# Performance work log

Hardware: AMD Instinct MI355X
Metric: run time of the kernel (lower is better)

## Reference

```python
import jax, jax.numpy as jnp
import numpy as np

N_PTS = 100000
C_IN, C_OUT, K = 16, 32, 3
B, D, H, W = 2, 32, 128, 128


def setup_inputs() -> dict:
    key = jax.random.key(0)
    kf, kw, kb, kz, ky, kx = jax.random.split(key, 6)
    features = jax.random.normal(kf, (N_PTS, C_IN), dtype=jnp.float32)
    coords = jnp.stack([
        jax.random.randint(kb, (N_PTS,), 0, B),
        jax.random.randint(kz, (N_PTS,), 0, D),
        jax.random.randint(ky, (N_PTS,), 0, H),
        jax.random.randint(kx, (N_PTS,), 0, W),
    ], axis=1).astype(jnp.int32)
    weight = jax.random.normal(kw, (K ** 3, C_IN, C_OUT), dtype=jnp.float32) * 0.01
    bias = jnp.zeros((C_OUT,), dtype=jnp.float32)
    return {"features": features, "coords": coords, "weight": weight, "bias": bias,
            "batch_size": B, "d_sp": D, "h_sp": H, "w_sp": W}


def reference(features, coords, weight, bias, batch_size, d_sp, h_sp, w_sp):
    # Scatter sparse voxel features into dense grid (B, C_in, D, H, W).
    n, c_in = features.shape
    c_out = weight.shape[2]
    k = K
    b, z, y, x = coords[:, 0], coords[:, 1], coords[:, 2], coords[:, 3]
    dense = jnp.zeros((batch_size, c_in, d_sp, h_sp, w_sp), dtype=features.dtype)
    dense = dense.at[b, :, z, y, x].set(features)  # (N,) advanced idx -> rows of (N, C_in)
    # Conv3d: torch copies weight.view(C_out, C_in, k, k, k) -> OIDHW kernel.
    kernel = weight.reshape(c_out, c_in, k, k, k)
    out = jax.lax.conv_general_dilated(
        dense, kernel,
        window_strides=(1, 1, 1),
        padding=[(1, 1), (1, 1), (1, 1)],
        dimension_numbers=("NCDHW", "OIDHW", "NCDHW"))
    out = jax.nn.relu(out + bias[None, :, None, None, None])
    # Dense equivalent of the torch nonzero-gather (which has data-dependent
    # shape): return the full dense activated grid (B, C_out, D, H, W).
    return out
```

## Files before the change

### kernel.cpp

```cpp
#include <hip/hip_runtime.h>

#define CIN   16
#define COUT  32
#define BATCH 2
#define DSP   32
#define HSP   128
#define WSP   128

#define TZ 4
#define TY 8
#define TX 16
#define NTZ 8
#define NTY 16
#define NTX 8
#define NTILES (BATCH*NTZ*NTY*NTX)
#define PZ 6
#define PY 10
#define PX 18
#define PVOX (PZ*PY*PX)
#define HALFU (PVOX*8)
#define BIN_CAP 128
#define NPAIR 14

typedef __bf16 bf16x8 __attribute__((ext_vector_type(8)));
typedef float  f32x4  __attribute__((ext_vector_type(4)));

__global__ void k_prep(const int4* __restrict__ coords, int n, int nbDedup,
                       int* __restrict__ map,
                       const float* __restrict__ w, __bf16* __restrict__ wpack) {
    if ((int)blockIdx.x < nbDedup) {
        int p = blockIdx.x * 256 + threadIdx.x;
        if (p >= n) return;
        int4 c = coords[p];
        int vox = ((c.x*DSP + c.y)*HSP + c.z)*WSP + c.w;
        atomicMax(&map[vox], p);
    } else {
        int i = (blockIdx.x - nbDedup) * 256 + threadIdx.x;
        if (i >= NPAIR*2*64*8) return;
        int j = i & 7, l = (i>>3) & 63, h = (i>>9) & 1, p = i >> 10;
        int tap = 2*p + ((l>>4)>>1);
        int co  = h*16 + (l & 15);
        int ci  = ((l>>4)&1)*8 + j;
        float v = (tap < 27) ? w[(co*CIN + ci)*27 + tap] : 0.0f;
        wpack[i] = (__bf16)v;
    }
}

__global__ void k_bin(const int4* __restrict__ coords, const int* __restrict__ map,
                      int* __restrict__ binCnt, int* __restrict__ bins, int n) {
    int p = blockIdx.x * 256 + threadIdx.x;
    if (p >= n) return;
    int4 c = coords[p];
    int vox = ((c.x*DSP + c.y)*HSP + c.z)*WSP + c.w;
    if (map[vox] != p) return;
    int tile = ((c.x*NTZ + (c.y>>2))*NTY + (c.z>>3))*NTX + (c.w>>4);
    int slot = atomicAdd(&binCnt[tile], 1);
    if (slot < BIN_CAP) bins[tile*BIN_CAP + slot] = p;
}

__global__ __launch_bounds__(256, 3) void k_conv(
    const float* __restrict__ feat, const int4* __restrict__ coords,
    const __bf16* __restrict__ wpack, const float* __restrict__ bias,
    const int* __restrict__ binCnt, const int* __restrict__ bins,
    float* __restrict__ out)
{
    __shared__ __align__(16) ushort patch[2*HALFU];
    __shared__ int ldsNt[27], ldsCnt[27], ldsPre[27];

    int tile = blockIdx.x;
    int txi = tile & 7;
    int tyi = (tile >> 3) & 15;
    int tzi = (tile >> 7) & 7;
    int b   = tile >> 10;
    int z0 = tzi*TZ, y0 = tyi*TY, x0 = txi*TX;

    int tid  = threadIdx.x;
    int lane = tid & 63, wave = tid >> 6;

    if (tid < 27) {
        int dz = tid/9 - 1, dy = (tid/3)%3 - 1, dx = tid%3 - 1;
        int nz = tzi+dz, ny = tyi+dy, nx = txi+dx;
        bool ok = (unsigned)nz < NTZ && (unsigned)ny < NTY && (unsigned)nx < NTX;
        int nt = ((b*NTZ + nz)*NTY + ny)*NTX + nx;
        ldsNt[tid]  = ok ? nt : 0;
        int c = ok ? binCnt[nt] : 0;
        ldsCnt[tid] = c > BIN_CAP ? BIN_CAP : c;
    }

    uint4* p4 = (uint4*)patch;
    for (int i = tid; i < 2*HALFU/8; i += 256) p4[i] = make_uint4(0,0,0,0);

    bf16x8 wf[NPAIR][2];
    #pragma unroll
    for (int p = 0; p < NPAIR; ++p)
        #pragma unroll
        for (int h = 0; h < 2; ++h)
            wf[p][h] = *(const bf16x8*)(wpack + ((size_t)((p*2 + h)*64 + lane))*8);

    int lx16  = lane & 15;
    int lhalf = (lane >> 4) & 1;
    int ltp   = (lane >> 4) >> 1;

    int voff[NPAIR];
    #pragma unroll
    for (int p = 0; p < NPAIR; ++p) {
        int tap = 2*p + ltp; if (tap > 26) tap = 26;
        int kd = tap/9, kh = (tap/3)%3, kw = tap%3;
        voff[p] = (kd*PY + kh)*PX + kw;
    }

    float bv0 = bias[lx16], bv1 = bias[16 + lx16];

    __syncthreads();

    if (tid < 32) {
        int c = (tid < 27) ? ldsCnt[tid] : 0;
        #pragma unroll
        for (int off = 1; off < 32; off <<= 1) {
            int nvl = __shfl_up(c, off);
            if (tid >= off) c += nvl;
        }
        if (tid < 27) ldsPre[tid] = c;
    }
    __syncthreads();

    int total = ldsPre[26];
    for (int i = tid; i < total; i += 256) {
        int lo = 0, hi = 26;
        #pragma unroll
        for (int it = 0; it < 5; ++it) {
            int mid = (lo + hi) >> 1;
            if (i < ldsPre[mid]) hi = mid; else lo = mid + 1;
        }
        int k = lo;
        int idx = i - (k ? ldsPre[k-1] : 0);
        int p = bins[ldsNt[k]*BIN_CAP + idx];
        int4 c = coords[p];
        int lz = c.y - z0 + 1, ly = c.z - y0 + 1, lx = c.w - x0 + 1;
        if ((unsigned)lz < PZ && (unsigned)ly < PY && (unsigned)lx < PX) {
            const float4* fp = (const float4*)(feat + (size_t)p*CIN);
            float4 f0 = fp[0], f1 = fp[1], f2 = fp[2], f3 = fp[3];
            bf16x8 vlo = { (__bf16)f0.x,(__bf16)f0.y,(__bf16)f0.z,(__bf16)f0.w,
                           (__bf16)f1.x,(__bf16)f1.y,(__bf16)f1.z,(__bf16)f1.w };
            bf16x8 vhi = { (__bf16)f2.x,(__bf16)f2.y,(__bf16)f2.z,(__bf16)f2.w,
                           (__bf16)f3.x,(__bf16)f3.y,(__bf16)f3.z,(__bf16)f3.w };
            int v = (lz*PY + ly)*PX + lx;
            *(bf16x8*)(patch + v*8)         = vlo;
            *(bf16x8*)(patch + HALFU + v*8) = vhi;
        }
    }
    __syncthreads();

    #pragma unroll 1
    for (int gi = 0; gi < 8; ++gi) {
        int g = wave*8 + gi;
        int z = g >> 3, y = g & 7;
        int laneVox = (z*PY + y)*PX + lx16;
        const ushort* pbase = patch + lhalf*HALFU + laneVox*8;
        f32x4 acc0 = {0.f,0.f,0.f,0.f}, acc1 = {0.f,0.f,0.f,0.f};
        #pragma unroll
        for (int p = 0; p < NPAIR; ++p) {
            bf16x8 a = *(const bf16x8*)(pbase + voff[p]*8);
            acc0 = __builtin_amdgcn_mfma_f32_16x16x32_bf16(a, wf[p][0], acc0, 0, 0, 0);
            acc1 = __builtin_amdgcn_mfma_f32_16x16x32_bf16(a, wf[p][1], acc1, 0, 0, 0);
        }
        int gz = z0 + z, gy = y0 + y, gx = x0 + ((lane >> 4) << 2);
        float4 o0, o1;
        o0.x = fmaxf(acc0[0]+bv0, 0.f); o0.y = fmaxf(acc0[1]+bv0, 0.f);
        o0.z = fmaxf(acc0[2]+bv0, 0.f); o0.w = fmaxf(acc0[3]+bv0, 0.f);
        o1.x = fmaxf(acc1[0]+bv1, 0.f); o1.y = fmaxf(acc1[1]+bv1, 0.f);
        o1.z = fmaxf(acc1[2]+bv1, 0.f); o1.w = fmaxf(acc1[3]+bv1, 0.f);
        size_t base0 = ((((size_t)b*COUT + lx16)*DSP + gz)*HSP + gy)*WSP + gx;
        size_t base1 = base0 + (size_t)16*DSP*HSP*WSP;
        *(float4*)(out + base0) = o0;
        *(float4*)(out + base1) = o1;
    }
}

extern "C" void kernel_launch(void* const* d_in, const int* in_sizes, int n_in,
                              void* d_out, int out_size, void* d_ws, size_t ws_size,
                              hipStream_t stream) {
    const float* feat   = (const float*)d_in[0];
    const int4*  coords = (const int4*)d_in[1];
    const float* weight = (const float*)d_in[2];
    const float* bias   = (const float*)d_in[3];
    float* out = (float*)d_out;
    int n = in_sizes[0] / CIN;

    int*    map    = (int*)d_ws;
    int*    binCnt = map + BATCH*DSP*HSP*WSP;
    int*    bins   = binCnt + NTILES;
    __bf16* wpack  = (__bf16*)(bins + NTILES*BIN_CAP);

    hipMemsetAsync(map, 0xFF, (size_t)BATCH*DSP*HSP*WSP*sizeof(int), stream);
    hipMemsetAsync(binCnt, 0, NTILES*sizeof(int), stream);

    int nb = (n + 255) / 256;
    int nbRepack = (NPAIR*2*64*8 + 255) / 256;
    k_prep<<<nb + nbRepack, 256, 0, stream>>>(coords, n, nb, map, weight, wpack);
    k_bin <<<nb, 256, 0, stream>>>(coords, map, binCnt, bins, n);
    k_conv<<<NTILES, 256, 0, stream>>>(feat, coords, wpack, bias, binCnt, bins, out);
}
```

Before: 79.41 us.

## Restructure conv loop for weight reuse, pack coords into bins, fold memset

Several changes at once. The conv kernel now keeps 8 row accumulators per wave and streams weights from global memory tap by tap with a one-step prefetch, instead of holding all weights in registers. It also raises the launch-bounds occupancy target and uses nontemporal output stores. The bins now carry packed coordinates alongside the point index, which removes the extra coords gather in conv. The binCnt memset is folded into the prep kernel to drop one API call. The cost is higher accumulator register pressure and repeated weight loads per block.

```diff
diff --git a/kernel.cpp b/kernel.cpp
--- a/kernel.cpp
+++ b/kernel.cpp
@@ -21,21 +21,25 @@
 #define HALFU (PVOX*8)
 #define BIN_CAP 128
 #define NPAIR 14
+#define NWREP ((NPAIR*2*64*8 + 255)/256)
+#define NZB   ((NTILES + 255)/256)
 
 typedef __bf16 bf16x8 __attribute__((ext_vector_type(8)));
 typedef float  f32x4  __attribute__((ext_vector_type(4)));
 
 __global__ void k_prep(const int4* __restrict__ coords, int n, int nbDedup,
                        int* __restrict__ map,
-                       const float* __restrict__ w, __bf16* __restrict__ wpack) {
-    if ((int)blockIdx.x < nbDedup) {
-        int p = blockIdx.x * 256 + threadIdx.x;
+                       const float* __restrict__ w, __bf16* __restrict__ wpack,
+                       int* __restrict__ binCnt) {
+    int bb = blockIdx.x;
+    if (bb < nbDedup) {
+        int p = bb * 256 + threadIdx.x;
         if (p >= n) return;
         int4 c = coords[p];
         int vox = ((c.x*DSP + c.y)*HSP + c.z)*WSP + c.w;
         atomicMax(&map[vox], p);
-    } else {
-        int i = (blockIdx.x - nbDedup) * 256 + threadIdx.x;
+    } else if (bb < nbDedup + NWREP) {
+        int i = (bb - nbDedup) * 256 + threadIdx.x;
         if (i >= NPAIR*2*64*8) return;
         int j = i & 7, l = (i>>3) & 63, h = (i>>9) & 1, p = i >> 10;
         int tap = 2*p + ((l>>4)>>1);
@@ -43,11 +47,14 @@
         int ci  = ((l>>4)&1)*8 + j;
         float v = (tap < 27) ? w[(co*CIN + ci)*27 + tap] : 0.0f;
         wpack[i] = (__bf16)v;
+    } else {
+        int i = (bb - nbDedup - NWREP) * 256 + threadIdx.x;
+        if (i < NTILES) binCnt[i] = 0;
     }
 }
 
 __global__ void k_bin(const int4* __restrict__ coords, const int* __restrict__ map,
-                      int* __restrict__ binCnt, int* __restrict__ bins, int n) {
+                      int* __restrict__ binCnt, int2* __restrict__ bins, int n) {
     int p = blockIdx.x * 256 + threadIdx.x;
     if (p >= n) return;
     int4 c = coords[p];
@@ -55,14 +62,14 @@
     if (map[vox] != p) return;
     int tile = ((c.x*NTZ + (c.y>>2))*NTY + (c.z>>3))*NTX + (c.w>>4);
     int slot = atomicAdd(&binCnt[tile], 1);
-    if (slot < BIN_CAP) bins[tile*BIN_CAP + slot] = p;
-}
-
-__global__ __launch_bounds__(256, 3) void k_conv(
-    const float* __restrict__ feat, const int4* __restrict__ coords,
-    const __bf16* __restrict__ wpack, const float* __restrict__ bias,
-    const int* __restrict__ binCnt, const int* __restrict__ bins,
-    float* __restrict__ out)
+    if (slot < BIN_CAP)
+        bins[tile*BIN_CAP + slot] = make_int2(p, (c.y<<14) | (c.z<<7) | c.w);
+}
+
+__global__ __launch_bounds__(256, 4) void k_conv(
+    const float* __restrict__ feat, const __bf16* __restrict__ wpack,
+    const float* __restrict__ bias, const int* __restrict__ binCnt,
+    const int2* __restrict__ bins, float* __restrict__ out)
 {
     __shared__ __align__(16) ushort patch[2*HALFU];
     __shared__ int ldsNt[27], ldsCnt[27], ldsPre[27];
@@ -90,13 +97,6 @@
     uint4* p4 = (uint4*)patch;
     for (int i = tid; i < 2*HALFU/8; i += 256) p4[i] = make_uint4(0,0,0,0);
 
-    bf16x8 wf[NPAIR][2];
-    #pragma unroll
-    for (int p = 0; p < NPAIR; ++p)
-        #pragma unroll
-        for (int h = 0; h < 2; ++h)
-            wf[p][h] = *(const bf16x8*)(wpack + ((size_t)((p*2 + h)*64 + lane))*8);
-
     int lx16  = lane & 15;
     int lhalf = (lane >> 4) & 1;
     int ltp   = (lane >> 4) >> 1;
@@ -125,6 +125,7 @@
     __syncthreads();
 
     int total = ldsPre[26];
+    #pragma unroll 2
     for (int i = tid; i < total; i += 256) {
         int lo = 0, hi = 26;
         #pragma unroll
@@ -134,11 +135,11 @@
         }
         int k = lo;
         int idx = i - (k ? ldsPre[k-1] : 0);
-        int p = bins[ldsNt[k]*BIN_CAP + idx];
-        int4 c = coords[p];
-        int lz = c.y - z0 + 1, ly = c.z - y0 + 1, lx = c.w - x0 + 1;
+        int2 e = bins[ldsNt[k]*BIN_CAP + idx];
+        int pz = e.y >> 14, py = (e.y >> 7) & 127, px = e.y & 127;
+        int lz = pz - z0 + 1, ly = py - y0 + 1, lx = px - x0 + 1;
         if ((unsigned)lz < PZ && (unsigned)ly < PY && (unsigned)lx < PX) {
-            const float4* fp = (const float4*)(feat + (size_t)p*CIN);
+            const float4* fp = (const float4*)(feat + (size_t)e.x*CIN);
             float4 f0 = fp[0], f1 = fp[1], f2 = fp[2], f3 = fp[3];
             bf16x8 vlo = { (__bf16)f0.x,(__bf16)f0.y,(__bf16)f0.z,(__bf16)f0.w,
                            (__bf16)f1.x,(__bf16)f1.y,(__bf16)f1.z,(__bf16)f1.w };
@@ -151,29 +152,42 @@
     }
     __syncthreads();
 
-    #pragma unroll 1
+    const ushort* pb = patch + lhalf*HALFU + ((wave*PY)*PX + lx16)*8;
+    f32x4 acc[8][2];
+    #pragma unroll
     for (int gi = 0; gi < 8; ++gi) {
-        int g = wave*8 + gi;
-        int z = g >> 3, y = g & 7;
-        int laneVox = (z*PY + y)*PX + lx16;
-        const ushort* pbase = patch + lhalf*HALFU + laneVox*8;
-        f32x4 acc0 = {0.f,0.f,0.f,0.f}, acc1 = {0.f,0.f,0.f,0.f};
+        acc[gi][0] = (f32x4){0.f,0.f,0.f,0.f};
+        acc[gi][1] = (f32x4){0.f,0.f,0.f,0.f};
+    }
+    bf16x8 w0 = *(const bf16x8*)(wpack + (size_t)(0*64 + lane)*8);
+    bf16x8 w1 = *(const bf16x8*)(wpack + (size_t)(1*64 + lane)*8);
+    #pragma unroll
+    for (int p = 0; p < NPAIR; ++p) {
+        int pn = (p + 1 < NPAIR) ? p + 1 : 0;
+        bf16x8 nw0 = *(const bf16x8*)(wpack + (size_t)((pn*2+0)*64 + lane)*8);
+        bf16x8 nw1 = *(const bf16x8*)(wpack + (size_t)((pn*2+1)*64 + lane)*8);
+        const ushort* pa = pb + voff[p]*8;
         #pragma unroll
-        for (int p = 0; p < NPAIR; ++p) {
-            bf16x8 a = *(const bf16x8*)(pbase + voff[p]*8);
-            acc0 = __builtin_amdgcn_mfma_f32_16x16x32_bf16(a, wf[p][0], acc0, 0, 0, 0);
-            acc1 = __builtin_amdgcn_mfma_f32_16x16x32_bf16(a, wf[p][1], acc1, 0, 0, 0);
-        }
-        int gz = z0 + z, gy = y0 + y, gx = x0 + ((lane >> 4) << 2);
-        float4 o0, o1;
-        o0.x = fmaxf(acc0[0]+bv0, 0.f); o0.y = fmaxf(acc0[1]+bv0, 0.f);
-        o0.z = fmaxf(acc0[2]+bv0, 0.f); o0.w = fmaxf(acc0[3]+bv0, 0.f);
-        o1.x = fmaxf(acc1[0]+bv1, 0.f); o1.y = fmaxf(acc1[1]+bv1, 0.f);
-        o1.z = fmaxf(acc1[2]+bv1, 0.f); o1.w = fmaxf(acc1[3]+bv1, 0.f);
+        for (int gi = 0; gi < 8; ++gi) {
+            bf16x8 a = *(const bf16x8*)(pa + gi*(PX*8));
+            acc[gi][0] = __builtin_amdgcn_mfma_f32_16x16x32_bf16(a, w0, acc[gi][0], 0,0,0);
+            acc[gi][1] = __builtin_amdgcn_mfma_f32_16x16x32_bf16(a, w1, acc[gi][1], 0,0,0);
+        }
+        w0 = nw0; w1 = nw1;
+    }
+
+    #pragma unroll
+    for (int gi = 0; gi < 8; ++gi) {
+        int gz = z0 + wave, gy = y0 + gi, gx = x0 + ((lane >> 4) << 2);
+        f32x4 o0, o1;
+        o0[0] = fmaxf(acc[gi][0][0]+bv0, 0.f); o0[1] = fmaxf(acc[gi][0][1]+bv0, 0.f);
+        o0[2] = fmaxf(acc[gi][0][2]+bv0, 0.f); o0[3] = fmaxf(acc[gi][0][3]+bv0, 0.f);
+        o1[0] = fmaxf(acc[gi][1][0]+bv1, 0.f); o1[1] = fmaxf(acc[gi][1][1]+bv1, 0.f);
+        o1[2] = fmaxf(acc[gi][1][2]+bv1, 0.f); o1[3] = fmaxf(acc[gi][1][3]+bv1, 0.f);
         size_t base0 = ((((size_t)b*COUT + lx16)*DSP + gz)*HSP + gy)*WSP + gx;
         size_t base1 = base0 + (size_t)16*DSP*HSP*WSP;
-        *(float4*)(out + base0) = o0;
-        *(float4*)(out + base1) = o1;
+        __builtin_nontemporal_store(o0, (f32x4*)(out + base0));
+        __builtin_nontemporal_store(o1, (f32x4*)(out + base1));
     }
 }
 
@@ -189,15 +203,13 @@
 
     int*    map    = (int*)d_ws;
     int*    binCnt = map + BATCH*DSP*HSP*WSP;
-    int*    bins   = binCnt + NTILES;
+    int2*   bins   = (int2*)(binCnt + NTILES);
     __bf16* wpack  = (__bf16*)(bins + NTILES*BIN_CAP);
 
     hipMemsetAsync(map, 0xFF, (size_t)BATCH*DSP*HSP*WSP*sizeof(int), stream);
-    hipMemsetAsync(binCnt, 0, NTILES*sizeof(int), stream);
 
     int nb = (n + 255) / 256;
-    int nbRepack = (NPAIR*2*64*8 + 255) / 256;
-    k_prep<<<nb + nbRepack, 256, 0, stream>>>(coords, n, nb, map, weight, wpack);
+    k_prep<<<nb + NWREP + NZB, 256, 0, stream>>>(coords, n, nb, map, weight, wpack, binCnt);
     k_bin <<<nb, 256, 0, stream>>>(coords, map, binCnt, bins, n);
-    k_conv<<<NTILES, 256, 0, stream>>>(feat, coords, wpack, bias, binCnt, bins, out);
-}
+    k_conv<<<NTILES, 256, 0, stream>>>(feat, wpack, bias, binCnt, bins, out);
+}
```

Result: faster. 75.34 us (-5.1%).
